# Kernel tuning notes

Measured on AMD Instinct MI355X. Metric: run time of the kernel, lower is better.

Reference implementation:

```python
import jax, jax.numpy as jnp
from jax import lax
import numpy as np

B, H, W, C, N = 4, 512, 512, 32, 300000
K, S, P, D = 3, 2, 1, 1  # kernel, stride, padding, dilation


def setup_inputs() -> dict:
    key = jax.random.key(0)
    kf, _ = jax.random.split(key)
    features = jax.random.normal(kf, (N, C), dtype=jnp.float32)
    # unique active coordinates (spconv requires unique sites)
    rng = np.random.default_rng(0)
    lin = rng.choice(B * H * W, size=N, replace=False)
    b = lin // (H * W)
    y = (lin // W) % H
    x = lin % W
    coors = jnp.asarray(np.stack([b, y, x], axis=1), dtype=jnp.int32)  # [N,3]
    return {"features": features, "coors": coors, "batch_size": B}


def reference(features, coors, batch_size):
    # Scatter active features onto a dense grid initialized to -inf so that
    # inputs only; outputs with no active input in window are inactive).
    neg_inf = jnp.array(-jnp.inf, dtype=features.dtype)
    dense = jnp.full((batch_size, H, W, features.shape[1]), neg_inf,
                     dtype=features.dtype)
    b, y, x = coors[:, 0], coors[:, 1], coors[:, 2]
    dense = dense.at[b, y, x].set(features)  # coords are unique
    out = lax.reduce_window(
        dense, neg_inf, lax.max,
        window_dimensions=(1, K, K, 1),
        window_strides=(1, S, S, 1),
        padding=((0, 0), (P, P), (P, P), (0, 0)),
        window_dilation=(1, D, D, 1))
    # inactive output sites -> 0 (dense view of the sparse output tensor)
    return jnp.where(jnp.isinf(out), jnp.zeros((), out.dtype), out)
```

## Files before the change

kernel.cpp:

```cpp
#include <hip/hip_runtime.h>
#include <math.h>

#define BB 4
#define HH 512
#define WW 512
#define CC 32
#define HO 256
#define WO 256

#define MAXOCC 96
#define OVFCAP 100

__global__ void fill_zero_kernel(int4* __restrict__ g, int n4) {
    int i = blockIdx.x * blockDim.x + threadIdx.x;
    if (i < n4) g[i] = make_int4(0, 0, 0, 0);
}

__global__ void scatter_idx_kernel(const int* __restrict__ coors,
                                   int* __restrict__ grid, int n) {
    int i = blockIdx.x * blockDim.x + threadIdx.x;
    if (i >= n) return;
    int b = coors[i * 3 + 0];
    int y = coors[i * 3 + 1];
    int x = coors[i * 3 + 2];
    grid[((size_t)b * HH + y) * WW + x] = i + 1;
}

__global__ void __launch_bounds__(256, 8)
pool_kernel(const float4* __restrict__ feat,
            const int* __restrict__ grid,
            float4* __restrict__ out) {
    int ox_base = (blockIdx.x & 7) * 32;
    int oy      = (blockIdx.x >> 3) & (HO - 1);
    int b       = blockIdx.x >> 11;

    int tid  = threadIdx.x;
    int lane = tid & 63;
    int cg   = tid & 7;
    int p    = tid >> 3;

    int iy0 = 2 * oy - 1;
    int gx0 = 2 * ox_base - 1;
    const int* gb = grid + (size_t)b * (HH * WW);

    __shared__ int    cnt;
    __shared__ int    smap[3 * 65];
    __shared__ int    srcidx[MAXOCC];
    __shared__ float4 sfeat[MAXOCC * 8];
    __shared__ int    ovf_c[OVFCAP];
    __shared__ int    ovf_i[OVFCAP];

    const float NEG = -INFINITY;
    if (tid == 0) cnt = 0;
    if (tid < 8) sfeat[tid] = make_float4(NEG, NEG, NEG, NEG);
    __syncthreads();

    {
        int v = 0;
        if (tid < 195) {
            int r = tid / 65;
            int c = tid - r * 65;
            int iy = iy0 + r;
            int gx = gx0 + c;
            if ((unsigned)iy < (unsigned)HH && (unsigned)gx < (unsigned)WW)
                v = gb[iy * WW + gx];
        }
        unsigned long long mask = __ballot(v != 0);
        int nz = (int)__popcll(mask);
        int base = 0;
        if (lane == 0 && nz) base = atomicAdd(&cnt, nz);
        base = __shfl(base, 0);
        int s = 1 + base + (int)__popcll(mask & ((1ull << lane) - 1ull));
        if (tid < 195) {
            int m = 0;
            if (v != 0) {
                if (s < MAXOCC) { srcidx[s] = v - 1; m = s; }
                else {
                    int o = s - MAXOCC;
                    ovf_c[o] = tid;
                    ovf_i[o] = v - 1;
                }
            }
            smap[tid] = m;
        }
    }
    __syncthreads();

    int hi = cnt < (MAXOCC - 1) ? cnt : (MAXOCC - 1);
    for (int s = 1 + (tid >> 3); s <= hi; s += 32)
        sfeat[(s << 3) + ((cg + s) & 7)] = feat[(size_t)srcidx[s] * 8 + cg];
    __syncthreads();

    int lc = 2 * p;
    float4 acc = make_float4(NEG, NEG, NEG, NEG);
#pragma unroll
    for (int r = 0; r < 3; ++r) {
        int m0 = smap[r * 65 + lc + 0];
        int m1 = smap[r * 65 + lc + 1];
        int m2 = smap[r * 65 + lc + 2];
        float4 f0 = sfeat[(m0 << 3) + ((cg + m0) & 7)];
        float4 f1 = sfeat[(m1 << 3) + ((cg + m1) & 7)];
        float4 f2 = sfeat[(m2 << 3) + ((cg + m2) & 7)];
        acc.x = fmaxf(fmaxf(acc.x, f0.x), fmaxf(f1.x, f2.x));
        acc.y = fmaxf(fmaxf(acc.y, f0.y), fmaxf(f1.y, f2.y));
        acc.z = fmaxf(fmaxf(acc.z, f0.z), fmaxf(f1.z, f2.z));
        acc.w = fmaxf(fmaxf(acc.w, f0.w), fmaxf(f1.w, f2.w));
    }

    if (cnt >= MAXOCC) {
        int novf = cnt - (MAXOCC - 1);
        if (novf > OVFCAP) novf = OVFCAP;
        for (int o = 0; o < novf; ++o) {
            int cell = ovf_c[o];
            int c = cell % 65;
            if (c >= lc && c <= lc + 2) {
                float4 fv = feat[(size_t)ovf_i[o] * 8 + cg];
                acc.x = fmaxf(acc.x, fv.x);
                acc.y = fmaxf(acc.y, fv.y);
                acc.z = fmaxf(acc.z, fv.z);
                acc.w = fmaxf(acc.w, fv.w);
            }
        }
    }

    acc.x = isinf(acc.x) ? 0.0f : acc.x;
    acc.y = isinf(acc.y) ? 0.0f : acc.y;
    acc.z = isinf(acc.z) ? 0.0f : acc.z;
    acc.w = isinf(acc.w) ? 0.0f : acc.w;

    size_t pos = ((size_t)(b * HO + oy) * WO + ox_base + p);
    out[pos * 8 + cg] = acc;
}

extern "C" void kernel_launch(void* const* d_in, const int* in_sizes, int n_in,
                              void* d_out, int out_size, void* d_ws, size_t ws_size,
                              hipStream_t stream) {
    const float* features = (const float*)d_in[0];
    const int*   coors    = (const int*)d_in[1];
    int n = in_sizes[0] / CC;

    int* grid = (int*)d_ws;

    {
        int n4 = (BB * HH * WW) / 4;
        int blk = 256, grd = (n4 + blk - 1) / blk;
        fill_zero_kernel<<<grd, blk, 0, stream>>>((int4*)grid, n4);
    }
    {
        int blk = 256, grd = (n + blk - 1) / blk;
        scatter_idx_kernel<<<grd, blk, 0, stream>>>(coors, grid, n);
    }
    {
        int grd = BB * HO * (WO / 32);
        pool_kernel<<<grd, 256, 0, stream>>>((const float4*)features, grid,
                                             (float4*)d_out);
    }
}
```

Baseline: 105.8 us.

## Load odd-column window cells directly from global instead of staging in LDS

Only even-column grid cells, which are shared between two neighbouring output windows, are now compacted into the LDS feature cache. Odd-column cells are used by a single output, so they are read straight from global memory into registers, with the grid index encoded as a negative map value. This shrinks the LDS staging work and the chance of overflowing the cache. The cost is three extra global loads per thread, issued unconditionally (index clamped to 0 when the cell is empty), and the overflow capacity is raised slightly.

```diff
diff --git a/kernel.cpp b/kernel.cpp
--- a/kernel.cpp
+++ b/kernel.cpp
@@ -9,7 +9,7 @@
 #define WO 256
 
 #define MAXOCC 96
-#define OVFCAP 100
+#define OVFCAP 104
 
 __global__ void fill_zero_kernel(int4* __restrict__ g, int n4) {
     int i = blockIdx.x * blockDim.x + threadIdx.x;
@@ -56,16 +56,17 @@
     __syncthreads();
 
     {
-        int v = 0;
+        int v = 0, c = 0;
         if (tid < 195) {
             int r = tid / 65;
-            int c = tid - r * 65;
+            c = tid - r * 65;
             int iy = iy0 + r;
             int gx = gx0 + c;
             if ((unsigned)iy < (unsigned)HH && (unsigned)gx < (unsigned)WW)
                 v = gb[iy * WW + gx];
         }
-        unsigned long long mask = __ballot(v != 0);
+        bool shared_cell = (v != 0) && ((c & 1) == 0);
+        unsigned long long mask = __ballot(shared_cell);
         int nz = (int)__popcll(mask);
         int base = 0;
         if (lane == 0 && nz) base = atomicAdd(&cnt, nz);
@@ -74,8 +75,11 @@
         if (tid < 195) {
             int m = 0;
             if (v != 0) {
-                if (s < MAXOCC) { srcidx[s] = v - 1; m = s; }
-                else {
+                if ((c & 1) != 0) {
+                    m = -v;
+                } else if (s < MAXOCC) {
+                    srcidx[s] = v - 1; m = s;
+                } else {
                     int o = s - MAXOCC;
                     ovf_c[o] = tid;
                     ovf_i[o] = v - 1;
@@ -92,19 +96,39 @@
     __syncthreads();
 
     int lc = 2 * p;
+    int m[9];
+#pragma unroll
+    for (int r = 0; r < 3; ++r) {
+        m[r * 3 + 0] = smap[r * 65 + lc + 0];
+        m[r * 3 + 1] = smap[r * 65 + lc + 1];
+        m[r * 3 + 2] = smap[r * 65 + lc + 2];
+    }
+
+    float4 fd[3];
+#pragma unroll
+    for (int r = 0; r < 3; ++r) {
+        int mv = m[r * 3 + 1];
+        int ridx = -mv - 1;
+        ridx = ridx < 0 ? 0 : ridx;
+        fd[r] = feat[(size_t)ridx * 8 + cg];
+    }
+
     float4 acc = make_float4(NEG, NEG, NEG, NEG);
 #pragma unroll
     for (int r = 0; r < 3; ++r) {
-        int m0 = smap[r * 65 + lc + 0];
-        int m1 = smap[r * 65 + lc + 1];
-        int m2 = smap[r * 65 + lc + 2];
+        int m0 = m[r * 3 + 0];
+        int m2 = m[r * 3 + 2];
         float4 f0 = sfeat[(m0 << 3) + ((cg + m0) & 7)];
-        float4 f1 = sfeat[(m1 << 3) + ((cg + m1) & 7)];
         float4 f2 = sfeat[(m2 << 3) + ((cg + m2) & 7)];
-        acc.x = fmaxf(fmaxf(acc.x, f0.x), fmaxf(f1.x, f2.x));
-        acc.y = fmaxf(fmaxf(acc.y, f0.y), fmaxf(f1.y, f2.y));
-        acc.z = fmaxf(fmaxf(acc.z, f0.z), fmaxf(f1.z, f2.z));
-        acc.w = fmaxf(fmaxf(acc.w, f0.w), fmaxf(f1.w, f2.w));
+        acc.x = fmaxf(acc.x, fmaxf(f0.x, f2.x));
+        acc.y = fmaxf(acc.y, fmaxf(f0.y, f2.y));
+        acc.z = fmaxf(acc.z, fmaxf(f0.z, f2.z));
+        acc.w = fmaxf(acc.w, fmaxf(f0.w, f2.w));
+        bool ok = m[r * 3 + 1] != 0;
+        acc.x = fmaxf(acc.x, ok ? fd[r].x : NEG);
+        acc.y = fmaxf(acc.y, ok ? fd[r].y : NEG);
+        acc.z = fmaxf(acc.z, ok ? fd[r].z : NEG);
+        acc.w = fmaxf(acc.w, ok ? fd[r].w : NEG);
     }
 
     if (cnt >= MAXOCC) {
```

After: 106.0 us. About the same (+0.2%).

## Stage only shared even-column cells in LDS, read private odd columns directly

Applied to the files above, without the earlier changes.

Window cells are split by column parity. Even input columns are shared between adjacent output pixels, so only those are staged in LDS, with fewer threads and smaller staging buffers. Each output pixel's own center (odd) column is now loaded straight from global memory into registers, and the gathered feature is masked when the cell is inactive. This halves LDS staging work and footprint, which may help occupancy, but adds unconditional global gathers per thread (row 0 used for empty cells) and shrinks the overflow capacity.

```diff
diff --git a/kernel.cpp b/kernel.cpp
--- a/kernel.cpp
+++ b/kernel.cpp
@@ -8,8 +8,8 @@
 #define HO 256
 #define WO 256
 
-#define MAXOCC 96
-#define OVFCAP 100
+#define MAXOCC 64
+#define OVFCAP 36
 
 __global__ void fill_zero_kernel(int4* __restrict__ g, int n4) {
     int i = blockIdx.x * blockDim.x + threadIdx.x;
@@ -43,42 +43,58 @@
     int gx0 = 2 * ox_base - 1;
     const int* gb = grid + (size_t)b * (HH * WW);
 
+    const float NEG = -INFINITY;
+
+    int cx = 2 * (ox_base + p);
+    int vc[3];
+#pragma unroll
+    for (int r = 0; r < 3; ++r) {
+        int iy = iy0 + r;
+        vc[r] = ((unsigned)iy < (unsigned)HH) ? gb[iy * WW + cx] : 0;
+    }
+    float4 fc[3];
+#pragma unroll
+    for (int r = 0; r < 3; ++r) {
+        int ridx = vc[r] - 1;
+        ridx = ridx < 0 ? 0 : ridx;
+        fc[r] = feat[(size_t)ridx * 8 + cg];
+    }
+
     __shared__ int    cnt;
-    __shared__ int    smap[3 * 65];
+    __shared__ int    smap[3 * 33];
     __shared__ int    srcidx[MAXOCC];
     __shared__ float4 sfeat[MAXOCC * 8];
     __shared__ int    ovf_c[OVFCAP];
     __shared__ int    ovf_i[OVFCAP];
 
-    const float NEG = -INFINITY;
     if (tid == 0) cnt = 0;
     if (tid < 8) sfeat[tid] = make_float4(NEG, NEG, NEG, NEG);
     __syncthreads();
 
     {
-        int v = 0;
-        if (tid < 195) {
-            int r = tid / 65;
-            int c = tid - r * 65;
+        int vs = 0;
+        if (tid < 99) {
+            int r  = tid / 33;
+            int c2 = tid - r * 33;
             int iy = iy0 + r;
-            int gx = gx0 + c;
+            int gx = gx0 + 2 * c2;
             if ((unsigned)iy < (unsigned)HH && (unsigned)gx < (unsigned)WW)
-                v = gb[iy * WW + gx];
+                vs = gb[iy * WW + gx];
         }
-        unsigned long long mask = __ballot(v != 0);
+        unsigned long long mask = __ballot(vs != 0);
         int nz = (int)__popcll(mask);
         int base = 0;
         if (lane == 0 && nz) base = atomicAdd(&cnt, nz);
         base = __shfl(base, 0);
         int s = 1 + base + (int)__popcll(mask & ((1ull << lane) - 1ull));
-        if (tid < 195) {
+        if (tid < 99) {
             int m = 0;
-            if (v != 0) {
-                if (s < MAXOCC) { srcidx[s] = v - 1; m = s; }
+            if (vs != 0) {
+                if (s < MAXOCC) { srcidx[s] = vs - 1; m = s; }
                 else {
                     int o = s - MAXOCC;
                     ovf_c[o] = tid;
-                    ovf_i[o] = v - 1;
+                    ovf_i[o] = vs - 1;
                 }
             }
             smap[tid] = m;
@@ -91,20 +107,22 @@
         sfeat[(s << 3) + ((cg + s) & 7)] = feat[(size_t)srcidx[s] * 8 + cg];
     __syncthreads();
 
-    int lc = 2 * p;
     float4 acc = make_float4(NEG, NEG, NEG, NEG);
 #pragma unroll
     for (int r = 0; r < 3; ++r) {
-        int m0 = smap[r * 65 + lc + 0];
-        int m1 = smap[r * 65 + lc + 1];
-        int m2 = smap[r * 65 + lc + 2];
+        int m0 = smap[r * 33 + p];
+        int m2 = smap[r * 33 + p + 1];
         float4 f0 = sfeat[(m0 << 3) + ((cg + m0) & 7)];
-        float4 f1 = sfeat[(m1 << 3) + ((cg + m1) & 7)];
         float4 f2 = sfeat[(m2 << 3) + ((cg + m2) & 7)];
-        acc.x = fmaxf(fmaxf(acc.x, f0.x), fmaxf(f1.x, f2.x));
-        acc.y = fmaxf(fmaxf(acc.y, f0.y), fmaxf(f1.y, f2.y));
-        acc.z = fmaxf(fmaxf(acc.z, f0.z), fmaxf(f1.z, f2.z));
-        acc.w = fmaxf(fmaxf(acc.w, f0.w), fmaxf(f1.w, f2.w));
+        acc.x = fmaxf(acc.x, fmaxf(f0.x, f2.x));
+        acc.y = fmaxf(acc.y, fmaxf(f0.y, f2.y));
+        acc.z = fmaxf(acc.z, fmaxf(f0.z, f2.z));
+        acc.w = fmaxf(acc.w, fmaxf(f0.w, f2.w));
+        bool ok = vc[r] != 0;
+        acc.x = fmaxf(acc.x, ok ? fc[r].x : NEG);
+        acc.y = fmaxf(acc.y, ok ? fc[r].y : NEG);
+        acc.z = fmaxf(acc.z, ok ? fc[r].z : NEG);
+        acc.w = fmaxf(acc.w, ok ? fc[r].w : NEG);
     }
 
     if (cnt >= MAXOCC) {
@@ -112,8 +130,8 @@
         if (novf > OVFCAP) novf = OVFCAP;
         for (int o = 0; o < novf; ++o) {
             int cell = ovf_c[o];
-            int c = cell % 65;
-            if (c >= lc && c <= lc + 2) {
+            int c2 = cell % 33;
+            if (c2 == p || c2 == p + 1) {
                 float4 fv = feat[(size_t)ovf_i[o] * 8 + cg];
                 acc.x = fmaxf(acc.x, fv.x);
                 acc.y = fmaxf(acc.y, fv.y);
```

New measurement: 108.2 us. +2.3%, slower.
